# Optimization experiments

Measured on AMD Instinct MI355X. Metric: run time of the kernel, lower is better.

Reference implementation:

```python
import jax, jax.numpy as jnp
import numpy as np

B, S, D, H = 8, 2048, 256, 4
DH = D // H
DFF = 4 * D


def setup_inputs() -> dict:
    key = jax.random.key(0)
    ks = jax.random.split(key, 32)
    w = lambda k, sh: (jax.random.normal(k, sh, jnp.float32) * 0.02)
    inp = {
        'global_feat': jax.random.normal(ks[0], (B, S, D), jnp.float32),
        'local_feat': jax.random.normal(ks[1], (B, S, D), jnp.float32),
        'text_feat': jax.random.normal(ks[2], (B, S, D), jnp.float32),
        'Wl1': w(ks[3], (D, D)), 'bl1': jnp.zeros((D,), jnp.float32),
        'Wl2': w(ks[4], (D, D)), 'bl2': jnp.zeros((D,), jnp.float32),
        'Wg': w(ks[5], (D, D)), 'bg': jnp.zeros((D,), jnp.float32),
        'Wgq': w(ks[6], (D, D)), 'bgq': jnp.zeros((D,), jnp.float32),
        'Wgk': w(ks[7], (D, D)), 'bgk': jnp.zeros((D,), jnp.float32),
        'Wgv': w(ks[8], (D, D)), 'bgv': jnp.zeros((D,), jnp.float32),
        'Wpq': w(ks[9], (D, D)), 'bpq': jnp.zeros((D,), jnp.float32),
        'Wpk': w(ks[10], (D, D)), 'bpk': jnp.zeros((D,), jnp.float32),
        'Wpv': w(ks[11], (D, D)), 'bpv': jnp.zeros((D,), jnp.float32),
        'Wd': w(ks[12], (D, D)), 'bd': jnp.zeros((D,), jnp.float32),
        'Wm1': w(ks[13], (D, DFF)), 'bm1': jnp.zeros((DFF,), jnp.float32),
        'Wm2': w(ks[14], (DFF, D)), 'bm2': jnp.zeros((D,), jnp.float32),
        'Wml': w(ks[15], (D, D)), 'bml': jnp.zeros((D,), jnp.float32),
    }
    return inp


def _heads(x):
    # [B,S,D] -> [B,H,S,DH]
    return x.reshape(B, S, H, DH).transpose(0, 2, 1, 3)


def _merge(x):
    # [B,H,S,DH] -> [B,S,D]
    return x.transpose(0, 2, 1, 3).reshape(B, S, D)


def reference(global_feat, local_feat, text_feat,
              Wl1, bl1, Wl2, bl2, Wg, bg,
              Wgq, bgq, Wgk, bgk, Wgv, bgv,
              Wpq, bpq, Wpk, bpk, Wpv, bpv,
              Wd, bd, Wm1, bm1, Wm2, bm2, Wml, bml):
    scale = 1.0 / jnp.sqrt(jnp.asarray(DH, jnp.float32))
    # embedding projections (dropout inactive in eval mode)
    dup_local = local_feat @ Wl1 + bl1      # local_embedding_1
    local = local_feat @ Wl2 + bl2          # local_embedding_2
    glob = global_feat @ Wg + bg            # global_embedding
    # global branch: Q from global, K/V from local
    gq = _heads(glob @ Wgq + bgq)
    gk = _heads(local @ Wgk + bgk)
    gv = _heads(local @ Wgv + bgv)
    # local branch: Q from duplicate local, K/V from text
    pq = _heads(dup_local @ Wpq + bpq)
    pk = _heads(text_feat @ Wpk + bpk)
    pv = _heads(text_feat @ Wpv + bpv)
    glb_probs = jax.nn.softmax(jnp.einsum('bhqd,bhkd->bhqk', gq, gk) * scale, axis=-1)
    plb_probs = jax.nn.softmax(jnp.einsum('bhqd,bhkd->bhqk', pq, pk) * scale, axis=-1)
    # bridging matmul: fuse probability maps
    plb_enhanced = jnp.einsum('bhqk,bhkl->bhql', glb_probs, plb_probs)
    glb_ctx = _merge(jnp.einsum('bhqk,bhkd->bhqd', glb_probs, gv))
    plb_ctx = _merge(jnp.einsum('bhqk,bhkd->bhqd', plb_enhanced, pv))
    out = (glb_ctx + plb_ctx) @ Wd + bd
    # GPT-style MLP (c_fc -> GELU -> c_proj)
    out = jax.nn.gelu(out @ Wm1 + bm1) @ Wm2 + bm2
    out = out @ Wml + bml
    return out
```

## Files before the change

kernel.cpp:

```cpp
#include <hip/hip_runtime.h>
#include <math.h>

#define Bn 8
#define Sn 2048
#define Dn 256
#define Hn 4
#define DHn 64
#define Mn (Bn*Sn)

typedef short bf16x8 __attribute__((ext_vector_type(8)));
typedef float f32x2  __attribute__((ext_vector_type(2)));
typedef float f32x4  __attribute__((ext_vector_type(4)));
typedef float f32x16 __attribute__((ext_vector_type(16)));
typedef int   i32x4  __attribute__((ext_vector_type(4)));
typedef unsigned short u16;
typedef unsigned int   u32;
typedef unsigned long long u64;

#if defined(__has_builtin)
#if __has_builtin(__builtin_amdgcn_global_load_lds)
#define HAVE_GLL 1
#endif
#if __has_builtin(__builtin_amdgcn_permlane32_swap)
#define HAVE_PLS 1
#endif
#endif
#ifndef HAVE_GLL
#define HAVE_GLL 0
#endif
#ifndef HAVE_PLS
#define HAVE_PLS 0
#endif

__device__ __forceinline__ u16 f2b(float f){
    u32 u = __float_as_uint(f);
    u32 r = (u + 0x7fffu + ((u >> 16) & 1u)) >> 16;
    return (u16)r;
}
__device__ __forceinline__ float b2f(u16 h){ return __uint_as_float(((u32)h) << 16); }
__device__ __forceinline__ u32 cvtpk(float lo, float hi){
    u32 r;
    asm("v_cvt_pk_bf16_f32 %0, %1, %2" : "=v"(r) : "v"(lo), "v"(hi));
    return r;
}

__device__ __forceinline__ float gelu_f(float x){
    const float K1 = 2.3021143113f;
    const float K2 = 0.1029390163f;
    float x2 = x * x;
    float arg = fmaf(x2 * x, K2, x * K1);
    float e = exp2f(arg);
    float r = __builtin_amdgcn_rcpf(e + 1.0f);
    return x - x * r;
}

struct WtArgs {
    const float* src[13];
    int kdim[13], ndim[13], dstoff[13], t0[13], rm[13];
};

__global__ __launch_bounds__(256) void prep_k(const float* __restrict__ lf, const float* __restrict__ gf,
                                              const float* __restrict__ tf,
                                              u16* __restrict__ o0, u16* __restrict__ o1, u16* __restrict__ o2,
                                              WtArgs a, u16* __restrict__ dst)
{
    __shared__ float tile[32][33];
    int bx = blockIdx.x;
    if (bx < 6144){
        int part = bx >> 11, blk = bx & 2047;
        const float* s = (part == 0) ? lf : (part == 1) ? gf : tf;
        u16* d = (part == 0) ? o0 : (part == 1) ? o1 : o2;
        size_t base = ((size_t)blk * 256 + threadIdx.x) * 8;
        float4 v0 = *(const float4*)(s + base);
        float4 v1 = *(const float4*)(s + base + 4);
        i32x4 o;
        o[0] = (int)cvtpk(v0.x, v0.y); o[1] = (int)cvtpk(v0.z, v0.w);
        o[2] = (int)cvtpk(v1.x, v1.y); o[3] = (int)cvtpk(v1.z, v1.w);
        *(i32x4*)(d + base) = o;
        return;
    }
    int tb = bx - 6144;
    int wi = 0;
    #pragma unroll
    for (int i = 1; i < 13; ++i) if (tb >= a.t0[i]) wi = i;
    int tt = tb - a.t0[wi];
    int N = a.ndim[wi], K = a.kdim[wi];
    int ntn = N >> 5;
    int tn = tt % ntn, tk = tt / ntn;
    int n0 = tn * 32, k0 = tk * 32;
    const float* src = a.src[wi];
    u16* out = dst + a.dstoff[wi];
    int r = threadIdx.x >> 5, c = threadIdx.x & 31;
    if (a.rm[wi]){
        #pragma unroll
        for (int rr = 0; rr < 4; ++rr){
            size_t idx = (size_t)(k0 + r*4 + rr) * N + n0 + c;
            out[idx] = f2b(src[idx]);
        }
        return;
    }
    #pragma unroll
    for (int rr = 0; rr < 4; ++rr)
        tile[r*4+rr][c] = src[(size_t)(k0 + r*4 + rr) * N + n0 + c];
    __syncthreads();
    #pragma unroll
    for (int rr = 0; rr < 4; ++rr)
        out[(size_t)(n0 + r*4 + rr) * K + k0 + c] = f2b(tile[c][r*4+rr]);
}

__global__ __launch_bounds__(256) void bcomb_k(const float* __restrict__ W2a, const float* __restrict__ W2b,
                                               const float* __restrict__ W2c, const float* __restrict__ W2d,
                                               const float* __restrict__ b1a, const float* __restrict__ b1b,
                                               const float* __restrict__ b1c, const float* __restrict__ b1d,
                                               const float* __restrict__ b2a, const float* __restrict__ b2b,
                                               const float* __restrict__ b2c, const float* __restrict__ b2d,
                                               float* __restrict__ fb)
{
    int p = blockIdx.x, a = threadIdx.x;
    const float* W2 = (p==0)?W2a:(p==1)?W2b:(p==2)?W2c:W2d;
    const float* b1 = (p==0)?b1a:(p==1)?b1b:(p==2)?b1c:b1d;
    const float* b2 = (p==0)?b2a:(p==1)?b2b:(p==2)?b2c:b2d;
    float s = b2[a];
    for (int j = 0; j < 256; ++j) s = fmaf(b1[j], W2[(size_t)j*256 + a], s);
    fb[p*256 + a] = s;
    if (p == 0) fb[1024 + a] = 0.f;
}

struct Grp {
    const u16* A[6];
    const u16* Wt[6];
    const float* bias[6];
    void* C[6];
    float scale[6];
};

template<int ACT, int OUTF32>
__global__ __launch_bounds__(256, 4) void gemm_k(Grp g, int N, int K)
{
    const u32 gx = gridDim.x, gy = gridDim.y;
    const u32 lgx = (u32)__builtin_ctz(gx);
    const u32 lgy = (u32)__builtin_ctz(gy);
    const u32 total = gx * gy * gridDim.z;
    const u32 lid = (blockIdx.z * gy + blockIdx.y) * gx + blockIdx.x;
    const u32 nl = (lid & 7) * (total >> 3) + (lid >> 3);
    const u32 bz = nl >> (lgx + lgy);
    const u32 by = (nl >> lgx) & (gy - 1);
    const u32 bx = nl & (gx - 1);

    const u16* __restrict__ A   = g.A[bz];
    const u16* __restrict__ Wt  = g.Wt[bz];
    const float* __restrict__ bias = g.bias[bz];
    void* __restrict__ Cv = g.C[bz];
    const float scale = g.scale[bz];

    __shared__ u16 sm[2][6144];
    const int tid = threadIdx.x;
    const int w = tid >> 6, lane = tid & 63;
    const int l15 = lane & 15, l4 = lane >> 4;
    const int wr = w & 1, wc = w >> 1;
    const int bm = by << 6, bn = bx << 7;
    const int xq = l4 ^ ((lane >> 1) & 3);

    f32x4 acc[4][2];
    #pragma unroll
    for (int nf = 0; nf < 4; ++nf)
        #pragma unroll
        for (int mf = 0; mf < 2; ++mf){
            acc[nf][mf][0]=0.f; acc[nf][mf][1]=0.f; acc[nf][mf][2]=0.f; acc[nf][mf][3]=0.f;
        }

    auto STAGE = [&](int buf, int kt){
        #pragma unroll
        for (int j = 0; j < 3; ++j){
            int ch = w*192 + j*64 + lane;
            int isB = ch >= 256;
            int cc  = isB ? ch - 256 : ch;
            int row = cc >> 2, q = cc & 3;
            int qs  = q ^ ((row >> 1) & 3);
            const u16* src = isB ? (Wt + (size_t)(bn + row) * K + kt + qs*8)
                                 : (A  + (size_t)(bm + row) * K + kt + qs*8);
#if HAVE_GLL
            u16* lb = &sm[buf][(size_t)(w*192 + j*64) * 8];
            __builtin_amdgcn_global_load_lds((const __attribute__((address_space(1))) void*)src,
                                             (__attribute__((address_space(3))) void*)lb, 16, 0, 0);
#else
            *(i32x4*)&sm[buf][(size_t)ch * 8] = *(const i32x4*)src;
#endif
        }
    };

    STAGE(0, 0);
    const int nk = K >> 5;
    for (int t = 0; t < nk; ++t){
        const int cur = t & 1;
        if (t + 1 < nk){
            STAGE(cur ^ 1, (t + 1) << 5);
#if HAVE_GLL
            asm volatile("s_waitcnt vmcnt(3)" ::: "memory");
#endif
        } else {
#if HAVE_GLL
            asm volatile("s_waitcnt vmcnt(0)" ::: "memory");
#endif
        }
        __builtin_amdgcn_s_barrier();
        asm volatile("" ::: "memory");

        const u16* As = sm[cur];
        const u16* Bs = sm[cur] + 2048;
        bf16x8 wf[4], af[2];
        #pragma unroll
        for (int nf = 0; nf < 4; ++nf)
            wf[nf] = *(const bf16x8*)(Bs + (size_t)(wc*64 + nf*16 + l15) * 32 + xq*8);
        #pragma unroll
        for (int mf = 0; mf < 2; ++mf)
            af[mf] = *(const bf16x8*)(As + (size_t)(wr*32 + mf*16 + l15) * 32 + xq*8);
        __builtin_amdgcn_s_setprio(1);
        #pragma unroll
        for (int nf = 0; nf < 4; ++nf)
            #pragma unroll
            for (int mf = 0; mf < 2; ++mf)
                acc[nf][mf] = __builtin_amdgcn_mfma_f32_16x16x32_bf16(wf[nf], af[mf], acc[nf][mf], 0, 0, 0);
        __builtin_amdgcn_s_setprio(0);

        asm volatile("" ::: "memory");
        __builtin_amdgcn_s_barrier();
    }

    #pragma unroll
    for (int nf = 0; nf < 4; ++nf){
        const int n0 = bn + wc*64 + nf*16 + l4*4;
        float4 b4 = *(const float4*)(bias + n0);
        #pragma unroll
        for (int mf = 0; mf < 2; ++mf){
            const int m = bm + wr*32 + mf*16 + l15;
            float r0 = (acc[nf][mf][0] + b4.x) * scale;
            float r1 = (acc[nf][mf][1] + b4.y) * scale;
            float r2 = (acc[nf][mf][2] + b4.z) * scale;
            float r3 = (acc[nf][mf][3] + b4.w) * scale;
            if (ACT){ r0 = gelu_f(r0); r1 = gelu_f(r1); r2 = gelu_f(r2); r3 = gelu_f(r3); }
            if (OUTF32){
                float4 o; o.x = r0; o.y = r1; o.z = r2; o.w = r3;
                *(float4*)((float*)Cv + (size_t)m * N + n0) = o;
            } else {
                u64 p = (u64)cvtpk(r0, r1) | ((u64)cvtpk(r2, r3) << 32);
                *(u64*)((u16*)Cv + (size_t)m * N + n0) = p;
            }
        }
    }
}

#define PSEL(idx, mm) ((((idx) >> 2) == 0) ? pp0[(4*((idx)&3)+(mm))>>1][(4*((idx)&3)+(mm))&1] \
                                           : pp1[(4*((idx)&3)+(mm))>>1][(4*((idx)&3)+(mm))&1])

template<int FUSE>
__global__ __launch_bounds__(256, 2) void attn_k(const u16* __restrict__ Q, const u16* __restrict__ Kp,
                                                 const u16* __restrict__ Vp, u16* __restrict__ O,
                                                 const u16* __restrict__ ADD)
{
    __shared__ u16 Kl[2][4608];
    __shared__ u16 Vt[2][4608];

    const int tid = threadIdx.x;
    const int w = tid >> 6, lane = tid & 63;
    const int c31 = lane & 31, h = lane >> 5;

    const int lid = blockIdx.x;
    const int nl = (lid & 7) * 64 + (lid >> 3);
    const int bh = nl >> 4;
    const int qb = (nl & 15) << 7;
    const size_t hb = (size_t)(bh >> 2) * Sn * Dn + (size_t)(bh & 3) * DHn;
    const int qrow = qb + w*32 + c31;

    bf16x8 qf[4];
    #pragma unroll
    for (int kc = 0; kc < 4; ++kc)
        qf[kc] = *(const bf16x8*)(Q + hb + (size_t)qrow * Dn + kc*16 + h*8);

    f32x16 ot0, ot1;
    #pragma unroll
    for (int r = 0; r < 16; ++r){ ot0[r] = 0.f; ot1[r] = 0.f; }
    float ll = 0.f;

    int koff0[4], koff1[4], voff0[4], voff1[4];
    #pragma unroll
    for (int kc = 0; kc < 4; ++kc){
        koff0[kc] = c31*72        + kc*16 + h*8;
        koff1[kc] = (32 + c31)*72 + kc*16 + h*8;
        voff0[kc] = koff0[kc];
        voff1[kc] = koff1[kc];
    }

    const int krow = tid >> 2, kq = tid & 3;
    const int vk0 = (tid & 15) * 4, vd0 = (tid >> 4) * 4;
    const u32 SEL_LO = 0x05040100u, SEL_HI = 0x07060302u;

    i32x4 kr0, kr1;
    u64 v0, v1, v2, v3;
    auto LOADKV = [&](int kt2){
        const u16* kb = Kp + hb + (size_t)(kt2 + krow) * Dn + kq*8;
        kr0 = *(const i32x4*)kb;
        kr1 = *(const i32x4*)(kb + 32);
        const u16* vb = Vp + hb + (size_t)(kt2 + vk0) * Dn + vd0;
        v0 = *(const u64*)(vb);
        v1 = *(const u64*)(vb + Dn);
        v2 = *(const u64*)(vb + 2*Dn);
        v3 = *(const u64*)(vb + 3*Dn);
    };
    auto WRITEKV = [&](int buf){
        *(i32x4*)&Kl[buf][(size_t)krow*72 + kq*8]      = kr0;
        *(i32x4*)&Kl[buf][(size_t)krow*72 + kq*8 + 32] = kr1;
        u32 a0 = (u32)v0, a1 = (u32)v1, a2 = (u32)v2, a3 = (u32)v3;
        u32 b0 = (u32)(v0 >> 32), b1 = (u32)(v1 >> 32), b2 = (u32)(v2 >> 32), b3 = (u32)(v3 >> 32);
        u64 wd0 = (u64)__builtin_amdgcn_perm(a1, a0, SEL_LO) | ((u64)__builtin_amdgcn_perm(a3, a2, SEL_LO) << 32);
        u64 wd1 = (u64)__builtin_amdgcn_perm(a1, a0, SEL_HI) | ((u64)__builtin_amdgcn_perm(a3, a2, SEL_HI) << 32);
        u64 wd2 = (u64)__builtin_amdgcn_perm(b1, b0, SEL_LO) | ((u64)__builtin_amdgcn_perm(b3, b2, SEL_LO) << 32);
        u64 wd3 = (u64)__builtin_amdgcn_perm(b1, b0, SEL_HI) | ((u64)__builtin_amdgcn_perm(b3, b2, SEL_HI) << 32);
        *(u64*)&Vt[buf][(size_t)(vd0 + 0)*72 + vk0] = wd0;
        *(u64*)&Vt[buf][(size_t)(vd0 + 1)*72 + vk0] = wd1;
        *(u64*)&Vt[buf][(size_t)(vd0 + 2)*72 + vk0] = wd2;
        *(u64*)&Vt[buf][(size_t)(vd0 + 3)*72 + vk0] = wd3;
    };

    LOADKV(0);
    WRITEKV(0);
    __syncthreads();

    #pragma unroll 2
    for (int t = 0; t < 32; ++t){
        const int c = t & 1;
        const bool more = (t < 31);
        if (more) LOADKV((t + 1) << 6);

        f32x16 s0, s1;
        #pragma unroll
        for (int r = 0; r < 16; ++r){ s0[r] = 0.f; s1[r] = 0.f; }
        __builtin_amdgcn_s_setprio(1);
        #pragma unroll
        for (int kc = 0; kc < 4; ++kc){
            bf16x8 k0 = *(const bf16x8*)&Kl[c][koff0[kc]];
            bf16x8 k1 = *(const bf16x8*)&Kl[c][koff1[kc]];
            s0 = __builtin_amdgcn_mfma_f32_32x32x16_bf16(k0, qf[kc], s0, 0, 0, 0);
            s1 = __builtin_amdgcn_mfma_f32_32x32x16_bf16(k1, qf[kc], s1, 0, 0, 0);
        }
        __builtin_amdgcn_s_setprio(0);

        f32x2 pp0[8], pp1[8];
        f32x2 rv = {0.f, 0.f};
        #pragma unroll
        for (int r = 0; r < 8; ++r){
            pp0[r][0] = exp2f(s0[2*r]); pp0[r][1] = exp2f(s0[2*r+1]);
            pp1[r][0] = exp2f(s1[2*r]); pp1[r][1] = exp2f(s1[2*r+1]);
            rv += pp0[r];
            rv += pp1[r];
        }
        ll += rv[0] + rv[1];

        __builtin_amdgcn_s_setprio(1);
        #pragma unroll
        for (int kc = 0; kc < 4; ++kc){
            const int iA = 2*kc, iB = 2*kc + 1;
            u32 wA0 = cvtpk(PSEL(iA,0), PSEL(iA,1));
            u32 wA1 = cvtpk(PSEL(iA,2), PSEL(iA,3));
            u32 wB0 = cvtpk(PSEL(iB,0), PSEL(iB,1));
            u32 wB1 = cvtpk(PSEL(iB,2), PSEL(iB,3));
            i32x4 pw;
#if HAVE_PLS
            {
                auto r02 = __builtin_amdgcn_permlane32_swap((int)wA0, (int)wB0, false, false);
                auto r13 = __builtin_amdgcn_permlane32_swap((int)wA1, (int)wB1, false, false);
                pw[0] = r02[0]; pw[1] = r13[0]; pw[2] = r02[1]; pw[3] = r13[1];
            }
#else
            {
                u32 s0v = h ? wA0 : wB0, s1v = h ? wA1 : wB1;
                u32 g0 = (u32)__shfl_xor((int)s0v, 32);
                u32 g1 = (u32)__shfl_xor((int)s1v, 32);
                pw[0] = (int)(h ? g0 : wA0);
                pw[1] = (int)(h ? g1 : wA1);
                pw[2] = (int)(h ? wB0 : g0);
                pw[3] = (int)(h ? wB1 : g1);
            }
#endif
            bf16x8 pb = *(bf16x8*)&pw;
            bf16x8 va  = *(const bf16x8*)&Vt[c][voff0[kc]];
            bf16x8 vb2 = *(const bf16x8*)&Vt[c][voff1[kc]];
            ot0 = __builtin_amdgcn_mfma_f32_32x32x16_bf16(va,  pb, ot0, 0, 0, 0);
            ot1 = __builtin_amdgcn_mfma_f32_32x32x16_bf16(vb2, pb, ot1, 0, 0, 0);
        }
        __builtin_amdgcn_s_setprio(0);

        if (more) WRITEKV(c ^ 1);
        __syncthreads();
    }

    ll += __shfl_xor(ll, 32);
    float inv = 1.0f / ll;
    #pragma unroll
    for (int rg = 0; rg < 4; ++rg){
        int d0 = 8*rg + 4*h;
        float r0 = ot0[4*rg+0]*inv, r1 = ot0[4*rg+1]*inv, r2 = ot0[4*rg+2]*inv, r3 = ot0[4*rg+3]*inv;
        float x0 = ot1[4*rg+0]*inv, x1 = ot1[4*rg+1]*inv, x2 = ot1[4*rg+2]*inv, x3 = ot1[4*rg+3]*inv;
        if (FUSE){
            u64 ga = *(const u64*)&ADD[hb + (size_t)qrow * Dn + d0];
            u64 gb = *(const u64*)&ADD[hb + (size_t)qrow * Dn + 32 + d0];
            r0 += b2f((u16)ga);         r1 += b2f((u16)(ga >> 16));
            r2 += b2f((u16)(ga >> 32)); r3 += b2f((u16)(ga >> 48));
            x0 += b2f((u16)gb);         x1 += b2f((u16)(gb >> 16));
            x2 += b2f((u16)(gb >> 32)); x3 += b2f((u16)(gb >> 48));
        }
        *(u64*)&O[hb + (size_t)qrow * Dn + d0]      = (u64)cvtpk(r0, r1) | ((u64)cvtpk(r2, r3) << 32);
        *(u64*)&O[hb + (size_t)qrow * Dn + 32 + d0] = (u64)cvtpk(x0, x1) | ((u64)cvtpk(x2, x3) << 32);
    }
}

extern "C" void kernel_launch(void* const* d_in, const int* in_sizes, int n_in,
                              void* d_out, int out_size, void* d_ws, size_t ws_size,
                              hipStream_t stream)
{
    (void)in_sizes; (void)n_in; (void)out_size; (void)ws_size;

    const float* gf  = (const float*)d_in[0];
    const float* lf  = (const float*)d_in[1];
    const float* tf  = (const float*)d_in[2];
    const float* Wl1 = (const float*)d_in[3];  const float* bl1 = (const float*)d_in[4];
    const float* Wl2 = (const float*)d_in[5];  const float* bl2 = (const float*)d_in[6];
    const float* Wg  = (const float*)d_in[7];  const float* bg  = (const float*)d_in[8];
    const float* Wgq = (const float*)d_in[9];  const float* bgq = (const float*)d_in[10];
    const float* Wgk = (const float*)d_in[11]; const float* bgk = (const float*)d_in[12];
    const float* Wgv = (const float*)d_in[13]; const float* bgv = (const float*)d_in[14];
    const float* Wpq = (const float*)d_in[15]; const float* bpq = (const float*)d_in[16];
    const float* bpk = (const float*)d_in[18];
    const float* bpv = (const float*)d_in[20];
    const float* bd  = (const float*)d_in[22];
    const float* bm1 = (const float*)d_in[24];
    const float* bm2 = (const float*)d_in[26];
    const float* bml = (const float*)d_in[28];

    const float C1 = 0.18033688011112042f;

    u16* ws = (u16*)d_ws;
    const size_t U = (size_t)Mn * Dn;
    u16* S[9];
    for (int i = 0; i < 9; ++i) S[i] = ws + (size_t)i * U;
    u16* wtb = ws + 9 * U;

    const int sq = 65536;
    u16* Wpqt = wtb + 0*sq;  u16* Wgqt = wtb + 1*sq;  u16* Wgkt = wtb + 2*sq;  u16* Wgvt = wtb + 3*sq;
    u16* Wpkt = wtb + 4*sq;  u16* Wpvt = wtb + 5*sq;  u16* Wdt  = wtb + 6*sq;  u16* Wmlt = wtb + 7*sq;
    u16* Wm1t = wtb + 524288;
    u16* Wm2t = wtb + 786432;
    u16* Wl1rm = wtb + 1048576;
    u16* Wl2rm = wtb + 1114112;
    u16* Wgrm  = wtb + 1179648;
    u16* Wcpqt = wtb + 1245184;
    u16* Wcgqt = wtb + 1310720;
    u16* Wcgkt = wtb + 1376256;
    u16* Wcgvt = wtb + 1441792;
    float* fb  = (float*)(wtb + 1507328);

    WtArgs wa;
    const float* wsrc[13] = {Wpq, Wgq, Wgk, Wgv, (const float*)d_in[17], (const float*)d_in[19],
                             (const float*)d_in[21], (const float*)d_in[27],
                             (const float*)d_in[23], (const float*)d_in[25], Wl1, Wl2, Wg};
    const int wdst[13] = {0, sq, 2*sq, 3*sq, 4*sq, 5*sq, 6*sq, 7*sq, 524288, 786432,
                          1048576, 1114112, 1179648};
    for (int i = 0; i < 13; ++i){
        wa.src[i] = wsrc[i];
        wa.kdim[i] = 256; wa.ndim[i] = 256;
        wa.dstoff[i] = wdst[i];
        wa.rm[i] = (i >= 10);
    }
    wa.ndim[8] = 1024;
    wa.kdim[9] = 1024;
    int acc_t = 0;
    for (int i = 0; i < 13; ++i){
        wa.t0[i] = acc_t;
        acc_t += (wa.ndim[i] >> 5) * (wa.kdim[i] >> 5);
    }
    prep_k<<<dim3(6144 + acc_t), 256, 0, stream>>>(lf, gf, tf, S[0], S[1], S[2], wa, wtb);

    bcomb_k<<<dim3(4), 256, 0, stream>>>(Wpq, Wgq, Wgk, Wgv, bl1, bg, bl2, bl2,
                                         bpq, bgq, bgk, bgv, fb);

    auto GN = [&](const Grp& g, int ng, int M, int N, int K, int act, int of32){
        dim3 gr(N / 128, M / 64, ng);
        if (act)        gemm_k<1,0><<<gr, 256, 0, stream>>>(g, N, K);
        else if (of32)  gemm_k<0,1><<<gr, 256, 0, stream>>>(g, N, K);
        else            gemm_k<0,0><<<gr, 256, 0, stream>>>(g, N, K);
    };
    auto G1 = [&](const u16* A, const u16* Wt_, const float* b, void* C, int N, int K,
                  float sc, int act, int of32){
        Grp g{};
        g.A[0] = A; g.Wt[0] = Wt_; g.bias[0] = b; g.C[0] = C; g.scale[0] = sc;
        GN(g, 1, Mn, N, K, act, of32);
    };

    {
        Grp g{};
        g.A[0] = Wpqt; g.Wt[0] = Wl1rm; g.bias[0] = fb + 1024; g.C[0] = Wcpqt; g.scale[0] = 1.f;
        g.A[1] = Wgqt; g.Wt[1] = Wgrm;  g.bias[1] = fb + 1024; g.C[1] = Wcgqt; g.scale[1] = 1.f;
        g.A[2] = Wgkt; g.Wt[2] = Wl2rm; g.bias[2] = fb + 1024; g.C[2] = Wcgkt; g.scale[2] = 1.f;
        g.A[3] = Wgvt; g.Wt[3] = Wl2rm; g.bias[3] = fb + 1024; g.C[3] = Wcgvt; g.scale[3] = 1.f;
        GN(g, 4, 256, 256, 256, 0, 0);
    }

    {
        Grp g{};
        g.A[0] = S[0]; g.Wt[0] = Wcpqt; g.bias[0] = fb + 0;   g.C[0] = S[3]; g.scale[0] = C1;
        g.A[1] = S[1]; g.Wt[1] = Wcgqt; g.bias[1] = fb + 256; g.C[1] = S[6]; g.scale[1] = C1;
        g.A[2] = S[0]; g.Wt[2] = Wcgkt; g.bias[2] = fb + 512; g.C[2] = S[7]; g.scale[2] = 1.f;
        g.A[3] = S[0]; g.Wt[3] = Wcgvt; g.bias[3] = fb + 768; g.C[3] = S[8]; g.scale[3] = 1.f;
        g.A[4] = S[2]; g.Wt[4] = Wpkt;  g.bias[4] = bpk;      g.C[4] = S[4]; g.scale[4] = 1.f;
        g.A[5] = S[2]; g.Wt[5] = Wpvt;  g.bias[5] = bpv;      g.C[5] = S[5]; g.scale[5] = 1.f;
        GN(g, 6, Mn, 256, 256, 0, 0);
    }

    attn_k<1><<<dim3(512), 256, 0, stream>>>(S[3], S[4], S[5], S[0], S[8]);
    attn_k<0><<<dim3(512), 256, 0, stream>>>(S[6], S[7], S[0], S[1], nullptr);

    G1(S[1], Wdt,  bd,  S[2], 256,  256,  1.f, 0, 0);
    G1(S[2], Wm1t, bm1, S[3], 1024, 256,  1.f, 1, 0);
    G1(S[3], Wm2t, bm2, S[7], 256,  1024, 1.f, 0, 0);
    G1(S[7], Wmlt, bml, d_out, 256, 256,  1.f, 0, 1);
}
```

Measured before the change: 225.8 us.

## Split attention key tiles across waves with LDS reduction; fold bias kernel into prep

Attention blocks now cover 64 query rows instead of 128, and the grid doubles to 1024 blocks. Within each block, wave pairs split every 64-key tile into two 32-key halves and combine their partial outputs and row sums through LDS at the end. Launch bounds rise to 4 blocks per CU, and the small bias-combination kernel is merged into prep_k as extra blocks so one launch disappears. The aim is more parallelism and occupancy for the attention kernels. The cost is that each K/V tile is loaded into LDS by twice as many blocks, plus a reduction step and a sync.

```diff
diff --git a/kernel.cpp b/kernel.cpp
--- a/kernel.cpp
+++ b/kernel.cpp
@@ -58,11 +58,18 @@
     const float* src[13];
     int kdim[13], ndim[13], dstoff[13], t0[13], rm[13];
 };
+struct BcArgs {
+    const float* W2[4];
+    const float* b1[4];
+    const float* b2[4];
+    float* fb;
+    int bc0;
+};
 
 __global__ __launch_bounds__(256) void prep_k(const float* __restrict__ lf, const float* __restrict__ gf,
                                               const float* __restrict__ tf,
                                               u16* __restrict__ o0, u16* __restrict__ o1, u16* __restrict__ o2,
-                                              WtArgs a, u16* __restrict__ dst)
+                                              WtArgs a, u16* __restrict__ dst, BcArgs bc)
 {
     __shared__ float tile[32][33];
     int bx = blockIdx.x;
@@ -79,6 +86,17 @@
         *(i32x4*)(d + base) = o;
         return;
     }
+    if (bx >= bc.bc0){
+        int p = bx - bc.bc0, aa = threadIdx.x;
+        const float* W2 = bc.W2[p];
+        const float* b1 = bc.b1[p];
+        const float* b2 = bc.b2[p];
+        float s = b2[aa];
+        for (int j = 0; j < 256; ++j) s = fmaf(b1[j], W2[(size_t)j*256 + aa], s);
+        bc.fb[p*256 + aa] = s;
+        if (p == 0) bc.fb[1024 + aa] = 0.f;
+        return;
+    }
     int tb = bx - 6144;
     int wi = 0;
     #pragma unroll
@@ -106,24 +124,6 @@
     #pragma unroll
     for (int rr = 0; rr < 4; ++rr)
         out[(size_t)(n0 + r*4 + rr) * K + k0 + c] = f2b(tile[c][r*4+rr]);
-}
-
-__global__ __launch_bounds__(256) void bcomb_k(const float* __restrict__ W2a, const float* __restrict__ W2b,
-                                               const float* __restrict__ W2c, const float* __restrict__ W2d,
-                                               const float* __restrict__ b1a, const float* __restrict__ b1b,
-                                               const float* __restrict__ b1c, const float* __restrict__ b1d,
-                                               const float* __restrict__ b2a, const float* __restrict__ b2b,
-                                               const float* __restrict__ b2c, const float* __restrict__ b2d,
-                                               float* __restrict__ fb)
-{
-    int p = blockIdx.x, a = threadIdx.x;
-    const float* W2 = (p==0)?W2a:(p==1)?W2b:(p==2)?W2c:W2d;
-    const float* b1 = (p==0)?b1a:(p==1)?b1b:(p==2)?b1c:b1d;
-    const float* b2 = (p==0)?b2a:(p==1)?b2b:(p==2)?b2c:b2d;
-    float s = b2[a];
-    for (int j = 0; j < 256; ++j) s = fmaf(b1[j], W2[(size_t)j*256 + a], s);
-    fb[p*256 + a] = s;
-    if (p == 0) fb[1024 + a] = 0.f;
 }
 
 struct Grp {
@@ -250,11 +250,8 @@
     }
 }
 
-#define PSEL(idx, mm) ((((idx) >> 2) == 0) ? pp0[(4*((idx)&3)+(mm))>>1][(4*((idx)&3)+(mm))&1] \
-                                           : pp1[(4*((idx)&3)+(mm))>>1][(4*((idx)&3)+(mm))&1])
-
 template<int FUSE>
-__global__ __launch_bounds__(256, 2) void attn_k(const u16* __restrict__ Q, const u16* __restrict__ Kp,
+__global__ __launch_bounds__(256, 4) void attn_k(const u16* __restrict__ Q, const u16* __restrict__ Kp,
                                                  const u16* __restrict__ Vp, u16* __restrict__ O,
                                                  const u16* __restrict__ ADD)
 {
@@ -264,13 +261,14 @@
     const int tid = threadIdx.x;
     const int w = tid >> 6, lane = tid & 63;
     const int c31 = lane & 31, h = lane >> 5;
+    const int qg = w & 1, kg = w >> 1;
 
     const int lid = blockIdx.x;
-    const int nl = (lid & 7) * 64 + (lid >> 3);
-    const int bh = nl >> 4;
-    const int qb = (nl & 15) << 7;
+    const int nl = (lid & 7) * 128 + (lid >> 3);
+    const int bh = nl >> 5;
+    const int qb = (nl & 31) << 6;
     const size_t hb = (size_t)(bh >> 2) * Sn * Dn + (size_t)(bh & 3) * DHn;
-    const int qrow = qb + w*32 + c31;
+    const int qrow = qb + qg*32 + c31;
 
     bf16x8 qf[4];
     #pragma unroll
@@ -282,13 +280,14 @@
     for (int r = 0; r < 16; ++r){ ot0[r] = 0.f; ot1[r] = 0.f; }
     float ll = 0.f;
 
-    int koff0[4], koff1[4], voff0[4], voff1[4];
-    #pragma unroll
-    for (int kc = 0; kc < 4; ++kc){
-        koff0[kc] = c31*72        + kc*16 + h*8;
-        koff1[kc] = (32 + c31)*72 + kc*16 + h*8;
-        voff0[kc] = koff0[kc];
-        voff1[kc] = koff1[kc];
+    int koff[4], voffA[2], voffB[2];
+    #pragma unroll
+    for (int kc = 0; kc < 4; ++kc)
+        koff[kc] = (kg*32 + c31)*72 + kc*16 + h*8;
+    #pragma unroll
+    for (int kcc = 0; kcc < 2; ++kcc){
+        voffA[kcc] = c31*72        + kg*32 + kcc*16 + h*8;
+        voffB[kcc] = (32 + c31)*72 + kg*32 + kcc*16 + h*8;
     }
 
     const int krow = tid >> 2, kq = tid & 3;
@@ -332,38 +331,33 @@
         const bool more = (t < 31);
         if (more) LOADKV((t + 1) << 6);
 
-        f32x16 s0, s1;
-        #pragma unroll
-        for (int r = 0; r < 16; ++r){ s0[r] = 0.f; s1[r] = 0.f; }
+        f32x16 s;
+        #pragma unroll
+        for (int r = 0; r < 16; ++r) s[r] = 0.f;
         __builtin_amdgcn_s_setprio(1);
         #pragma unroll
         for (int kc = 0; kc < 4; ++kc){
-            bf16x8 k0 = *(const bf16x8*)&Kl[c][koff0[kc]];
-            bf16x8 k1 = *(const bf16x8*)&Kl[c][koff1[kc]];
-            s0 = __builtin_amdgcn_mfma_f32_32x32x16_bf16(k0, qf[kc], s0, 0, 0, 0);
-            s1 = __builtin_amdgcn_mfma_f32_32x32x16_bf16(k1, qf[kc], s1, 0, 0, 0);
+            bf16x8 k0 = *(const bf16x8*)&Kl[c][koff[kc]];
+            s = __builtin_amdgcn_mfma_f32_32x32x16_bf16(k0, qf[kc], s, 0, 0, 0);
         }
         __builtin_amdgcn_s_setprio(0);
 
-        f32x2 pp0[8], pp1[8];
+        f32x2 pp[8];
         f32x2 rv = {0.f, 0.f};
         #pragma unroll
         for (int r = 0; r < 8; ++r){
-            pp0[r][0] = exp2f(s0[2*r]); pp0[r][1] = exp2f(s0[2*r+1]);
-            pp1[r][0] = exp2f(s1[2*r]); pp1[r][1] = exp2f(s1[2*r+1]);
-            rv += pp0[r];
-            rv += pp1[r];
+            pp[r][0] = exp2f(s[2*r]); pp[r][1] = exp2f(s[2*r+1]);
+            rv += pp[r];
         }
         ll += rv[0] + rv[1];
 
         __builtin_amdgcn_s_setprio(1);
         #pragma unroll
-        for (int kc = 0; kc < 4; ++kc){
-            const int iA = 2*kc, iB = 2*kc + 1;
-            u32 wA0 = cvtpk(PSEL(iA,0), PSEL(iA,1));
-            u32 wA1 = cvtpk(PSEL(iA,2), PSEL(iA,3));
-            u32 wB0 = cvtpk(PSEL(iB,0), PSEL(iB,1));
-            u32 wB1 = cvtpk(PSEL(iB,2), PSEL(iB,3));
+        for (int kcc = 0; kcc < 2; ++kcc){
+            u32 wA0 = cvtpk(pp[4*kcc+0][0], pp[4*kcc+0][1]);
+            u32 wA1 = cvtpk(pp[4*kcc+1][0], pp[4*kcc+1][1]);
+            u32 wB0 = cvtpk(pp[4*kcc+2][0], pp[4*kcc+2][1]);
+            u32 wB1 = cvtpk(pp[4*kcc+3][0], pp[4*kcc+3][1]);
             i32x4 pw;
 #if HAVE_PLS
             {
@@ -383,8 +377,8 @@
             }
 #endif
             bf16x8 pb = *(bf16x8*)&pw;
-            bf16x8 va  = *(const bf16x8*)&Vt[c][voff0[kc]];
-            bf16x8 vb2 = *(const bf16x8*)&Vt[c][voff1[kc]];
+            bf16x8 va  = *(const bf16x8*)&Vt[c][voffA[kcc]];
+            bf16x8 vb2 = *(const bf16x8*)&Vt[c][voffB[kcc]];
             ot0 = __builtin_amdgcn_mfma_f32_32x32x16_bf16(va,  pb, ot0, 0, 0, 0);
             ot1 = __builtin_amdgcn_mfma_f32_32x32x16_bf16(vb2, pb, ot1, 0, 0, 0);
         }
@@ -395,6 +389,23 @@
     }
 
     ll += __shfl_xor(ll, 32);
+    float* red  = (float*)&Kl[0][0];
+    float* redL = red + 2*64*34;
+    if (kg == 1){
+        float* base = red + (size_t)(qg*64 + lane)*34;
+        #pragma unroll
+        for (int r = 0; r < 16; ++r){ base[r] = ot0[r]; base[16+r] = ot1[r]; }
+        if (h == 0) redL[qg*32 + c31] = ll;
+    }
+    __syncthreads();
+    if (kg == 1) return;
+    {
+        float* base = red + (size_t)(qg*64 + lane)*34;
+        #pragma unroll
+        for (int r = 0; r < 16; ++r){ ot0[r] += base[r]; ot1[r] += base[16+r]; }
+        ll += redL[qg*32 + c31];
+    }
+
     float inv = 1.0f / ll;
     #pragma unroll
     for (int rg = 0; rg < 4; ++rg){
@@ -478,10 +489,12 @@
         wa.t0[i] = acc_t;
         acc_t += (wa.ndim[i] >> 5) * (wa.kdim[i] >> 5);
     }
-    prep_k<<<dim3(6144 + acc_t), 256, 0, stream>>>(lf, gf, tf, S[0], S[1], S[2], wa, wtb);
-
-    bcomb_k<<<dim3(4), 256, 0, stream>>>(Wpq, Wgq, Wgk, Wgv, bl1, bg, bl2, bl2,
-                                         bpq, bgq, bgk, bgv, fb);
+    BcArgs bc;
+    bc.W2[0] = Wpq; bc.W2[1] = Wgq; bc.W2[2] = Wgk; bc.W2[3] = Wgv;
+    bc.b1[0] = bl1; bc.b1[1] = bg;  bc.b1[2] = bl2; bc.b1[3] = bl2;
+    bc.b2[0] = bpq; bc.b2[1] = bgq; bc.b2[2] = bgk; bc.b2[3] = bgv;
+    bc.fb = fb; bc.bc0 = 6144 + acc_t;
+    prep_k<<<dim3(6144 + acc_t + 4), 256, 0, stream>>>(lf, gf, tf, S[0], S[1], S[2], wa, wtb, bc);
 
     auto GN = [&](const Grp& g, int ng, int M, int N, int K, int act, int of32){
         dim3 gr(N / 128, M / 64, ng);
@@ -516,8 +529,8 @@
         GN(g, 6, Mn, 256, 256, 0, 0);
     }
 
-    attn_k<1><<<dim3(512), 256, 0, stream>>>(S[3], S[4], S[5], S[0], S[8]);
-    attn_k<0><<<dim3(512), 256, 0, stream>>>(S[6], S[7], S[0], S[1], nullptr);
+    attn_k<1><<<dim3(1024), 256, 0, stream>>>(S[3], S[4], S[5], S[0], S[8]);
+    attn_k<0><<<dim3(1024), 256, 0, stream>>>(S[6], S[7], S[0], S[1], nullptr);
 
     G1(S[1], Wdt,  bd,  S[2], 256,  256,  1.f, 0, 0);
     G1(S[2], Wm1t, bm1, S[3], 1024, 256,  1.f, 1, 0);
```

New measurement: 262.6 us. +16.3%, slower.

## Load attention K fragments directly into registers and fold bias-combine into prep kernel

Applied to the files above, without the earlier changes.

The attention kernel stops staging K tiles through shared memory. Each lane now loads its K MFMA fragments straight from global memory into registers, with the next tile prefetched after the QK MFMAs. This removes the K LDS writes and reads and halves LDS usage, at the cost of more VGPRs and uncoalesced global reads that may rely on L2 hits. Separately, the small bias-combine kernel is merged into the prep kernel as four extra blocks, which saves one launch.

```diff
diff --git a/kernel.cpp b/kernel.cpp
--- a/kernel.cpp
+++ b/kernel.cpp
@@ -58,11 +58,19 @@
     const float* src[13];
     int kdim[13], ndim[13], dstoff[13], t0[13], rm[13];
 };
+struct BcArgs {
+    const float* W2[4];
+    const float* b1[4];
+    const float* b2[4];
+    int off[4];
+    float* fb;
+    int bc0;
+};
 
 __global__ __launch_bounds__(256) void prep_k(const float* __restrict__ lf, const float* __restrict__ gf,
                                               const float* __restrict__ tf,
                                               u16* __restrict__ o0, u16* __restrict__ o1, u16* __restrict__ o2,
-                                              WtArgs a, u16* __restrict__ dst)
+                                              WtArgs a, u16* __restrict__ dst, BcArgs bc)
 {
     __shared__ float tile[32][33];
     int bx = blockIdx.x;
@@ -79,6 +87,17 @@
         *(i32x4*)(d + base) = o;
         return;
     }
+    if (bx >= bc.bc0){
+        int p = bx - bc.bc0, aa = threadIdx.x;
+        const float* W2 = bc.W2[p];
+        const float* b1 = bc.b1[p];
+        const float* b2 = bc.b2[p];
+        float s = b2[aa];
+        for (int j = 0; j < 256; ++j) s = fmaf(b1[j], W2[(size_t)j*256 + aa], s);
+        bc.fb[bc.off[p] + aa] = s;
+        if (p == 0) bc.fb[1024 + aa] = 0.f;
+        return;
+    }
     int tb = bx - 6144;
     int wi = 0;
     #pragma unroll
@@ -106,24 +125,6 @@
     #pragma unroll
     for (int rr = 0; rr < 4; ++rr)
         out[(size_t)(n0 + r*4 + rr) * K + k0 + c] = f2b(tile[c][r*4+rr]);
-}
-
-__global__ __launch_bounds__(256) void bcomb_k(const float* __restrict__ W2a, const float* __restrict__ W2b,
-                                               const float* __restrict__ W2c, const float* __restrict__ W2d,
-                                               const float* __restrict__ b1a, const float* __restrict__ b1b,
-                                               const float* __restrict__ b1c, const float* __restrict__ b1d,
-                                               const float* __restrict__ b2a, const float* __restrict__ b2b,
-                                               const float* __restrict__ b2c, const float* __restrict__ b2d,
-                                               float* __restrict__ fb)
-{
-    int p = blockIdx.x, a = threadIdx.x;
-    const float* W2 = (p==0)?W2a:(p==1)?W2b:(p==2)?W2c:W2d;
-    const float* b1 = (p==0)?b1a:(p==1)?b1b:(p==2)?b1c:b1d;
-    const float* b2 = (p==0)?b2a:(p==1)?b2b:(p==2)?b2c:b2d;
-    float s = b2[a];
-    for (int j = 0; j < 256; ++j) s = fmaf(b1[j], W2[(size_t)j*256 + a], s);
-    fb[p*256 + a] = s;
-    if (p == 0) fb[1024 + a] = 0.f;
 }
 
 struct Grp {
@@ -250,15 +251,11 @@
     }
 }
 
-#define PSEL(idx, mm) ((((idx) >> 2) == 0) ? pp0[(4*((idx)&3)+(mm))>>1][(4*((idx)&3)+(mm))&1] \
-                                           : pp1[(4*((idx)&3)+(mm))>>1][(4*((idx)&3)+(mm))&1])
-
 template<int FUSE>
 __global__ __launch_bounds__(256, 2) void attn_k(const u16* __restrict__ Q, const u16* __restrict__ Kp,
                                                  const u16* __restrict__ Vp, u16* __restrict__ O,
                                                  const u16* __restrict__ ADD)
 {
-    __shared__ u16 Kl[2][4608];
     __shared__ u16 Vt[2][4608];
 
     const int tid = threadIdx.x;
@@ -282,34 +279,36 @@
     for (int r = 0; r < 16; ++r){ ot0[r] = 0.f; ot1[r] = 0.f; }
     float ll = 0.f;
 
-    int koff0[4], koff1[4], voff0[4], voff1[4];
+    int voff0[4], voff1[4];
     #pragma unroll
     for (int kc = 0; kc < 4; ++kc){
-        koff0[kc] = c31*72        + kc*16 + h*8;
-        koff1[kc] = (32 + c31)*72 + kc*16 + h*8;
-        voff0[kc] = koff0[kc];
-        voff1[kc] = koff1[kc];
-    }
-
-    const int krow = tid >> 2, kq = tid & 3;
+        voff0[kc] = c31*72        + kc*16 + h*8;
+        voff1[kc] = (32 + c31)*72 + kc*16 + h*8;
+    }
+
     const int vk0 = (tid & 15) * 4, vd0 = (tid >> 4) * 4;
     const u32 SEL_LO = 0x05040100u, SEL_HI = 0x07060302u;
 
-    i32x4 kr0, kr1;
+    bf16x8 kr0[4], kr1[4];
+    auto LOADK = [&](int kt2){
+        const u16* kb  = Kp + hb + (size_t)(kt2 + c31) * Dn + h*8;
+        const u16* kb2 = kb + 32 * Dn;
+        #pragma unroll
+        for (int kc = 0; kc < 4; ++kc){
+            kr0[kc] = *(const bf16x8*)(kb  + kc*16);
+            kr1[kc] = *(const bf16x8*)(kb2 + kc*16);
+        }
+    };
+
     u64 v0, v1, v2, v3;
-    auto LOADKV = [&](int kt2){
-        const u16* kb = Kp + hb + (size_t)(kt2 + krow) * Dn + kq*8;
-        kr0 = *(const i32x4*)kb;
-        kr1 = *(const i32x4*)(kb + 32);
+    auto LOADV = [&](int kt2){
         const u16* vb = Vp + hb + (size_t)(kt2 + vk0) * Dn + vd0;
         v0 = *(const u64*)(vb);
         v1 = *(const u64*)(vb + Dn);
         v2 = *(const u64*)(vb + 2*Dn);
         v3 = *(const u64*)(vb + 3*Dn);
     };
-    auto WRITEKV = [&](int buf){
-        *(i32x4*)&Kl[buf][(size_t)krow*72 + kq*8]      = kr0;
-        *(i32x4*)&Kl[buf][(size_t)krow*72 + kq*8 + 32] = kr1;
+    auto WRITEV = [&](int buf){
         u32 a0 = (u32)v0, a1 = (u32)v1, a2 = (u32)v2, a3 = (u32)v3;
         u32 b0 = (u32)(v0 >> 32), b1 = (u32)(v1 >> 32), b2 = (u32)(v2 >> 32), b3 = (u32)(v3 >> 32);
         u64 wd0 = (u64)__builtin_amdgcn_perm(a1, a0, SEL_LO) | ((u64)__builtin_amdgcn_perm(a3, a2, SEL_LO) << 32);
@@ -322,15 +321,16 @@
         *(u64*)&Vt[buf][(size_t)(vd0 + 3)*72 + vk0] = wd3;
     };
 
-    LOADKV(0);
-    WRITEKV(0);
+    LOADK(0);
+    LOADV(0);
+    WRITEV(0);
     __syncthreads();
 
     #pragma unroll 2
     for (int t = 0; t < 32; ++t){
         const int c = t & 1;
         const bool more = (t < 31);
-        if (more) LOADKV((t + 1) << 6);
+        if (more) LOADV((t + 1) << 6);
 
         f32x16 s0, s1;
         #pragma unroll
@@ -338,12 +338,12 @@
         __builtin_amdgcn_s_setprio(1);
         #pragma unroll
         for (int kc = 0; kc < 4; ++kc){
-            bf16x8 k0 = *(const bf16x8*)&Kl[c][koff0[kc]];
-            bf16x8 k1 = *(const bf16x8*)&Kl[c][koff1[kc]];
-            s0 = __builtin_amdgcn_mfma_f32_32x32x16_bf16(k0, qf[kc], s0, 0, 0, 0);
-            s1 = __builtin_amdgcn_mfma_f32_32x32x16_bf16(k1, qf[kc], s1, 0, 0, 0);
+            s0 = __builtin_amdgcn_mfma_f32_32x32x16_bf16(kr0[kc], qf[kc], s0, 0, 0, 0);
+            s1 = __builtin_amdgcn_mfma_f32_32x32x16_bf16(kr1[kc], qf[kc], s1, 0, 0, 0);
         }
         __builtin_amdgcn_s_setprio(0);
+
+        if (more) LOADK((t + 1) << 6);
 
         f32x2 pp0[8], pp1[8];
         f32x2 rv = {0.f, 0.f};
@@ -360,10 +360,18 @@
         #pragma unroll
         for (int kc = 0; kc < 4; ++kc){
             const int iA = 2*kc, iB = 2*kc + 1;
-            u32 wA0 = cvtpk(PSEL(iA,0), PSEL(iA,1));
-            u32 wA1 = cvtpk(PSEL(iA,2), PSEL(iA,3));
-            u32 wB0 = cvtpk(PSEL(iB,0), PSEL(iB,1));
-            u32 wB1 = cvtpk(PSEL(iB,2), PSEL(iB,3));
+            u32 wA0, wA1, wB0, wB1;
+            if (kc < 2){
+                wA0 = cvtpk(pp0[iA*2+0][0], pp0[iA*2+0][1]);
+                wA1 = cvtpk(pp0[iA*2+1][0], pp0[iA*2+1][1]);
+                wB0 = cvtpk(pp0[iB*2+0][0], pp0[iB*2+0][1]);
+                wB1 = cvtpk(pp0[iB*2+1][0], pp0[iB*2+1][1]);
+            } else {
+                wA0 = cvtpk(pp1[(iA-4)*2+0][0], pp1[(iA-4)*2+0][1]);
+                wA1 = cvtpk(pp1[(iA-4)*2+1][0], pp1[(iA-4)*2+1][1]);
+                wB0 = cvtpk(pp1[(iB-4)*2+0][0], pp1[(iB-4)*2+0][1]);
+                wB1 = cvtpk(pp1[(iB-4)*2+1][0], pp1[(iB-4)*2+1][1]);
+            }
             i32x4 pw;
 #if HAVE_PLS
             {
@@ -390,7 +398,7 @@
         }
         __builtin_amdgcn_s_setprio(0);
 
-        if (more) WRITEKV(c ^ 1);
+        if (more) WRITEV(c ^ 1);
         __syncthreads();
     }
 
@@ -435,7 +443,7 @@
     const float* bd  = (const float*)d_in[22];
     const float* bm1 = (const float*)d_in[24];
     const float* bm2 = (const float*)d_in[26];
-    const float* bml = (const float*)d_in[28];
+    const float* Wml = (const float*)d_in[27]; const float* bml = (const float*)d_in[28];
 
     const float C1 = 0.18033688011112042f;
 
@@ -448,8 +456,8 @@
     const int sq = 65536;
     u16* Wpqt = wtb + 0*sq;  u16* Wgqt = wtb + 1*sq;  u16* Wgkt = wtb + 2*sq;  u16* Wgvt = wtb + 3*sq;
     u16* Wpkt = wtb + 4*sq;  u16* Wpvt = wtb + 5*sq;  u16* Wdt  = wtb + 6*sq;  u16* Wmlt = wtb + 7*sq;
-    u16* Wm1t = wtb + 524288;
-    u16* Wm2t = wtb + 786432;
+    u16* Wm1t  = wtb + 524288;
+    u16* Wm2t  = wtb + 786432;
     u16* Wl1rm = wtb + 1048576;
     u16* Wl2rm = wtb + 1114112;
     u16* Wgrm  = wtb + 1179648;
@@ -461,7 +469,7 @@
 
     WtArgs wa;
     const float* wsrc[13] = {Wpq, Wgq, Wgk, Wgv, (const float*)d_in[17], (const float*)d_in[19],
-                             (const float*)d_in[21], (const float*)d_in[27],
+                             (const float*)d_in[21], Wml,
                              (const float*)d_in[23], (const float*)d_in[25], Wl1, Wl2, Wg};
     const int wdst[13] = {0, sq, 2*sq, 3*sq, 4*sq, 5*sq, 6*sq, 7*sq, 524288, 786432,
                           1048576, 1114112, 1179648};
@@ -478,10 +486,13 @@
         wa.t0[i] = acc_t;
         acc_t += (wa.ndim[i] >> 5) * (wa.kdim[i] >> 5);
     }
-    prep_k<<<dim3(6144 + acc_t), 256, 0, stream>>>(lf, gf, tf, S[0], S[1], S[2], wa, wtb);
-
-    bcomb_k<<<dim3(4), 256, 0, stream>>>(Wpq, Wgq, Wgk, Wgv, bl1, bg, bl2, bl2,
-                                         bpq, bgq, bgk, bgv, fb);
+    BcArgs bc;
+    bc.W2[0] = Wpq; bc.W2[1] = Wgq; bc.W2[2] = Wgk; bc.W2[3] = Wgv;
+    bc.b1[0] = bl1; bc.b1[1] = bg;  bc.b1[2] = bl2; bc.b1[3] = bl2;
+    bc.b2[0] = bpq; bc.b2[1] = bgq; bc.b2[2] = bgk; bc.b2[3] = bgv;
+    bc.off[0] = 0; bc.off[1] = 256; bc.off[2] = 512; bc.off[3] = 768;
+    bc.fb = fb; bc.bc0 = 6144 + acc_t;
+    prep_k<<<dim3(6144 + acc_t + 4), 256, 0, stream>>>(lf, gf, tf, S[0], S[1], S[2], wa, wtb, bc);
 
     auto GN = [&](const Grp& g, int ng, int M, int N, int K, int act, int of32){
         dim3 gr(N / 128, M / 64, ng);
@@ -489,11 +500,11 @@
         else if (of32)  gemm_k<0,1><<<gr, 256, 0, stream>>>(g, N, K);
         else            gemm_k<0,0><<<gr, 256, 0, stream>>>(g, N, K);
     };
-    auto G1 = [&](const u16* A, const u16* Wt_, const float* b, void* C, int N, int K,
+    auto G1 = [&](const u16* A, const u16* Wt_, const float* b, void* C, int M, int N, int K,
                   float sc, int act, int of32){
         Grp g{};
         g.A[0] = A; g.Wt[0] = Wt_; g.bias[0] = b; g.C[0] = C; g.scale[0] = sc;
-        GN(g, 1, Mn, N, K, act, of32);
+        GN(g, 1, M, N, K, act, of32);
     };
 
     {
@@ -519,8 +530,8 @@
     attn_k<1><<<dim3(512), 256, 0, stream>>>(S[3], S[4], S[5], S[0], S[8]);
     attn_k<0><<<dim3(512), 256, 0, stream>>>(S[6], S[7], S[0], S[1], nullptr);
 
-    G1(S[1], Wdt,  bd,  S[2], 256,  256,  1.f, 0, 0);
-    G1(S[2], Wm1t, bm1, S[3], 1024, 256,  1.f, 1, 0);
-    G1(S[3], Wm2t, bm2, S[7], 256,  1024, 1.f, 0, 0);
-    G1(S[7], Wmlt, bml, d_out, 256, 256,  1.f, 0, 1);
-}
+    G1(S[1], Wdt,  bd,  S[2],  Mn, 256,  256,  1.f, 0, 0);
+    G1(S[2], Wm1t, bm1, S[3],  Mn, 1024, 256,  1.f, 1, 0);
+    G1(S[3], Wm2t, bm2, S[7],  Mn, 256,  1024, 1.f, 0, 0);
+    G1(S[7], Wmlt, bml, d_out, Mn, 256,  256,  1.f, 0, 1);
+}
```

After: 297.6 us. 31.8% more time.
